# Performance work log

Measured on AMD Instinct MI355X. Metric: run time of the kernel, lower is better.

## Reference

```python
import jax, jax.numpy as jnp
import numpy as np
from math import ceil, log2

LEVELS = 8
# pywt 'db4' filters (length 8)
DB4_DEC_HI = np.array([-0.23037781330885523, 0.7148465705525415, -0.6308807679295904,
                       -0.02798376941698385, 0.18703481171888114, 0.030841381835986965,
                       -0.032883011666982945, -0.010597401784997278], dtype=np.float32)
DB4_REC_HI = np.array([-0.010597401784997278, -0.032883011666982945, 0.030841381835986965,
                       0.18703481171888114, -0.02798376941698385, -0.6308807679295904,
                       0.7148465705525415, -0.23037781330885523], dtype=np.float32)


def setup_inputs() -> dict:
    key = jax.random.key(0)
    x = jax.random.normal(key, (2048, 3000), dtype=jnp.float32)
    scaling = jnp.tile(jnp.asarray(DB4_DEC_HI), (LEVELS, 1))       # [levels, 8]
    scaling_rec = jnp.tile(jnp.asarray(DB4_REC_HI), (LEVELS, 1))   # [levels, 8]
    return {"input": x, "scaling": scaling, "scaling_rec": scaling_rec}


def _make_wavelet(h):
    # g = flip(h); g[1::2] *= -1
    g = jnp.flip(h, axis=-1)
    signs = jnp.where(jnp.arange(g.shape[-1]) % 2 == 1, -1.0, 1.0).astype(g.dtype)
    return g * signs


def _circ_conv(x, filt, transpose=False):
    # FFT-based circular convolution (filter zero-padded to input length)
    L = x.shape[-1]
    ra = jnp.fft.rfft(x)
    rb = jnp.fft.rfft(filt, n=L)
    if transpose:
        rb = jnp.conj(rb)
    return jnp.fft.irfft(ra * rb, n=L)


def _upsample2(x):
    # interleave zeros: out[:, ::2] = x
    n, k = x.shape
    out = jnp.zeros((n, 2 * k), dtype=x.dtype)
    return out.at[:, ::2].set(x)


def _forward(x, scaling, scaling_rec):
    levels = scaling.shape[0]
    m = x.shape[1]
    L = 2 ** ceil(log2(m))
    p0 = (L - m) // 2
    p1 = ceil((L - m) / 2)
    x = jnp.pad(x, ((0, 0), (p0, p1)), mode="edge")  # ReplicationPad1d

    approx = x
    wav_coeffs = []
    for lvl in range(levels):
        wavelet = _make_wavelet(scaling_rec[lvl])
        details = _circ_conv(approx, wavelet)[:, ::2]
        approx = _circ_conv(approx, scaling[lvl])[:, ::2]
        wav_coeffs.append(details)
    wav_coeffs.append(approx)

    # (no thresholding: the original forward copies coeffs unmodified)
    filtered = list(wav_coeffs)
    approx = filtered[-1]
    for lvl in reversed(range(levels)):
        details = filtered[lvl]
        wav_syn = _make_wavelet(scaling_rec[lvl])
        d_rec = _circ_conv(_upsample2(details), wav_syn, transpose=True)
        a_rec = _circ_conv(_upsample2(approx), scaling[lvl], transpose=True)
        approx = d_rec + a_rec

    recon = approx[:, p0:m + p1]
    coeffs = jnp.concatenate(wav_coeffs, axis=-1)  # total length == L
    return recon, coeffs


def reference(input, scaling, scaling_rec):
    return _forward(input, scaling, scaling_rec)
```

## Files before the change

### kernel.cpp

```cpp
#include <hip/hip_runtime.h>

#define NROWS 2048
#define MLEN  3000
#define LPAD  4096
#define PAD0  548
#define NLVL  8
#define NT    256

__global__ __launch_bounds__(NT) void despawn_kernel(
    const float* __restrict__ x,
    const float* __restrict__ scaling,
    const float* __restrict__ scaling_rec,
    float* __restrict__ recon_out,
    float* __restrict__ coef_out)
{
    __shared__ float SA[LPAD];
    __shared__ float SB[LPAD / 2];
    __shared__ float fsca[NLVL * 8];
    __shared__ float fwav[NLVL * 8];

    const int tid = threadIdx.x;
    const int row = blockIdx.x;
    float* const crow = coef_out + (size_t)row * LPAD;

    if (tid < NLVL * 8) {
        const int lvl = tid >> 3, k = tid & 7;
        fsca[tid] = scaling[tid];
        fwav[tid] = scaling_rec[lvl * 8 + (7 - k)] * ((k & 1) ? -1.0f : 1.0f);
    }

    const float* xr = x + (size_t)row * MLEN;
    for (int i = tid; i < LPAD; i += NT) {
        int j = i - PAD0;
        j = j < 0 ? 0 : (j > MLEN - 1 ? MLEN - 1 : j);
        SA[((i & 1) ? (LPAD / 2) : 0) + (i >> 1)] = xr[j];
    }
    __syncthreads();

    float* cur = SA;
    float* alt = SB;
    int M = LPAD;
    int coff = 0;
    for (int lvl = 0; lvl < NLVL; ++lvl) {
        const int H = M >> 1;
        const int hm = H - 1;
        const float* we = &fwav[lvl * 8];
        const float* se = &fsca[lvl * 8];
        const float* ev = cur;
        const float* od = cur + H;
        for (int j = tid; j < H; j += NT) {
            float ds = 0.0f, as = 0.0f;
#pragma unroll
            for (int m = 0; m < 4; ++m) {
                const float vE = ev[(j - m) & hm];
                const float vO = od[(j - m - 1) & hm];
                ds = fmaf(vE, we[2 * m], ds);
                ds = fmaf(vO, we[2 * m + 1], ds);
                as = fmaf(vE, se[2 * m], as);
                as = fmaf(vO, se[2 * m + 1], as);
            }
            crow[coff + j] = ds;
            alt[((j & 1) ? (H >> 1) : 0) + (j >> 1)] = as;
        }
        __syncthreads();
        coff += H;
        float* t = cur; cur = alt; alt = t;
        M = H;
    }
    if (tid < 16) {
        const float v = cur[((tid & 1) ? 8 : 0) + (tid >> 1)];
        crow[LPAD - 16 + tid] = v;
        SA[16 + tid] = v;
    }
    __syncthreads();

    const float* a = SA + 16;
    int len = 16;
    float* obuf = SB;
    for (int lvl = NLVL - 1; lvl >= 0; --lvl) {
        const int Mout = len << 1;
        const int lmask = len - 1;
        const float* d = crow + (LPAD - (LPAD >> lvl));
        const float* we = &fwav[lvl * 8];
        const float* se = &fsca[lvl * 8];
        for (int n = tid; n < Mout; n += NT) {
            const int p = n & 1;
            const int i0 = (n + p) >> 1;
            float sum = 0.0f;
#pragma unroll
            for (int m = 0; m < 4; ++m) {
                const int idx = (i0 + m) & lmask;
                sum = fmaf(d[idx], we[p + 2 * m], sum);
                sum = fmaf(a[idx], se[p + 2 * m], sum);
            }
            obuf[n] = sum;
        }
        __syncthreads();
        a = obuf;
        len = Mout;
        obuf = (obuf == SB) ? SA : SB;
    }

    float* ro = recon_out + (size_t)row * MLEN;
    for (int i = tid; i < MLEN; i += NT) ro[i] = a[PAD0 + i];
}

extern "C" void kernel_launch(void* const* d_in, const int* in_sizes, int n_in,
                              void* d_out, int out_size, void* d_ws, size_t ws_size,
                              hipStream_t stream) {
    const float* x           = (const float*)d_in[0];
    const float* scaling     = (const float*)d_in[1];
    const float* scaling_rec = (const float*)d_in[2];
    float* recon = (float*)d_out;
    float* coefo = recon + (size_t)NROWS * MLEN;
    despawn_kernel<<<dim3(NROWS), dim3(NT), 0, stream>>>(x, scaling, scaling_rec,
                                                         recon, coefo);
    (void)in_sizes; (void)n_in; (void)out_size; (void)d_ws; (void)ws_size;
}
```

Measured before the change: 113.8 us.

## Vectorize wavelet levels with float4 and cache coarse details in LDS

The input load, each analysis level and each synthesis level now work on four or eight outputs per thread using float4 loads and stores, with the filter taps held in registers. Detail coefficients for levels 3 and above are also kept in a shared-memory buffer, so synthesis reads them from LDS rather than from global memory. The last synthesis level writes straight to the recon output with vectorized stores, dropping the extra staging pass. The aim is fewer LDS and global transactions and less per-element index arithmetic, at the cost of more registers and an extra 2KB of LDS per block.

```diff
diff --git a/kernel.cpp b/kernel.cpp
--- a/kernel.cpp
+++ b/kernel.cpp
@@ -6,6 +6,8 @@
 #define PAD0  548
 #define NLVL  8
 #define NT    256
+
+union F4 { float4 v; float f[4]; };
 
 __global__ __launch_bounds__(NT) void despawn_kernel(
     const float* __restrict__ x,
@@ -14,95 +16,185 @@
     float* __restrict__ recon_out,
     float* __restrict__ coef_out)
 {
-    __shared__ float SA[LPAD];
-    __shared__ float SB[LPAD / 2];
-    __shared__ float fsca[NLVL * 8];
-    __shared__ float fwav[NLVL * 8];
+    __shared__ __align__(16) float SA[LPAD];
+    __shared__ __align__(16) float SB[LPAD / 2];
+    __shared__ __align__(16) float CS[512];
+    __shared__ float fsca[64];
+    __shared__ float fwav[64];
 
     const int tid = threadIdx.x;
     const int row = blockIdx.x;
     float* const crow = coef_out + (size_t)row * LPAD;
 
-    if (tid < NLVL * 8) {
+    if (tid < 64) {
         const int lvl = tid >> 3, k = tid & 7;
         fsca[tid] = scaling[tid];
         fwav[tid] = scaling_rec[lvl * 8 + (7 - k)] * ((k & 1) ? -1.0f : 1.0f);
     }
 
     const float* xr = x + (size_t)row * MLEN;
-    for (int i = tid; i < LPAD; i += NT) {
-        int j = i - PAD0;
-        j = j < 0 ? 0 : (j > MLEN - 1 ? MLEN - 1 : j);
-        SA[((i & 1) ? (LPAD / 2) : 0) + (i >> 1)] = xr[j];
+    const float xlo = xr[0], xhi = xr[MLEN - 1];
+    {
+        const float4* xr4 = reinterpret_cast<const float4*>(xr);
+        for (int g = tid; g < MLEN / 4; g += NT) {
+            F4 u; u.v = xr4[g];
+            const int h = PAD0 / 2 + 2 * g;
+            *reinterpret_cast<float2*>(&SA[h])            = make_float2(u.f[0], u.f[2]);
+            *reinterpret_cast<float2*>(&SA[LPAD / 2 + h]) = make_float2(u.f[1], u.f[3]);
+        }
+    }
+    for (int i = tid; i < PAD0 / 2; i += NT) {
+        SA[i] = xlo;
+        SA[LPAD / 2 + i] = xlo;
+        SA[PAD0 / 2 + MLEN / 2 + i] = xhi;
+        SA[LPAD / 2 + PAD0 / 2 + MLEN / 2 + i] = xhi;
     }
     __syncthreads();
 
-    float* cur = SA;
-    float* alt = SB;
-    int M = LPAD;
-    int coff = 0;
-    for (int lvl = 0; lvl < NLVL; ++lvl) {
-        const int H = M >> 1;
-        const int hm = H - 1;
-        const float* we = &fwav[lvl * 8];
-        const float* se = &fsca[lvl * 8];
-        const float* ev = cur;
-        const float* od = cur + H;
-        for (int j = tid; j < H; j += NT) {
-            float ds = 0.0f, as = 0.0f;
-#pragma unroll
-            for (int m = 0; m < 4; ++m) {
-                const float vE = ev[(j - m) & hm];
-                const float vO = od[(j - m - 1) & hm];
-                ds = fmaf(vE, we[2 * m], ds);
-                ds = fmaf(vO, we[2 * m + 1], ds);
-                as = fmaf(vE, se[2 * m], as);
-                as = fmaf(vO, se[2 * m + 1], as);
-            }
-            crow[coff + j] = ds;
-            alt[((j & 1) ? (H >> 1) : 0) + (j >> 1)] = as;
-        }
-        __syncthreads();
-        coff += H;
-        float* t = cur; cur = alt; alt = t;
-        M = H;
-    }
+    {
+        float* cur = SA;
+        float* alt = SB;
+        int H = LPAD / 2;
+        int coff = 0;
+        for (int lvl = 0; lvl < NLVL; ++lvl) {
+            float W[8], S[8];
+#pragma unroll
+            for (int k = 0; k < 8; ++k) { W[k] = fwav[lvl * 8 + k]; S[k] = fsca[lvl * 8 + k]; }
+            const int q = H >> 2;
+            const int qm = q - 1;
+            const float4* ev4 = reinterpret_cast<const float4*>(cur);
+            const float4* od4 = reinterpret_cast<const float4*>(cur + H);
+            float4* dst4 = reinterpret_cast<float4*>(crow + coff);
+            float4* cs4 = (lvl >= 3) ? reinterpret_cast<float4*>(&CS[coff - 3584]) : nullptr;
+            for (int t = tid; t < q; t += NT) {
+                F4 Ea, Eb, Oa, Ob;
+                Ea.v = ev4[(t - 1) & qm];
+                Eb.v = ev4[t];
+                Oa.v = od4[(t - 1) & qm];
+                Ob.v = od4[t];
+                float e[8] = {Ea.f[0],Ea.f[1],Ea.f[2],Ea.f[3],Eb.f[0],Eb.f[1],Eb.f[2],Eb.f[3]};
+                float o[8] = {Oa.f[0],Oa.f[1],Oa.f[2],Oa.f[3],Ob.f[0],Ob.f[1],Ob.f[2],Ob.f[3]};
+                float ds[4], as[4];
+#pragma unroll
+                for (int u = 0; u < 4; ++u) {
+                    float d = 0.f, a = 0.f;
+#pragma unroll
+                    for (int m = 0; m < 4; ++m) {
+                        const float vE = e[4 + u - m];
+                        const float vO = o[3 + u - m];
+                        d = fmaf(vE, W[2 * m], d);
+                        d = fmaf(vO, W[2 * m + 1], d);
+                        a = fmaf(vE, S[2 * m], a);
+                        a = fmaf(vO, S[2 * m + 1], a);
+                    }
+                    ds[u] = d; as[u] = a;
+                }
+                F4 dv; dv.f[0] = ds[0]; dv.f[1] = ds[1]; dv.f[2] = ds[2]; dv.f[3] = ds[3];
+                dst4[t] = dv.v;
+                if (cs4) cs4[t] = dv.v;
+                *reinterpret_cast<float2*>(alt + 2 * t)            = make_float2(as[0], as[2]);
+                *reinterpret_cast<float2*>(alt + (H >> 1) + 2 * t) = make_float2(as[1], as[3]);
+            }
+            __syncthreads();
+            coff += H;
+            float* tmp = cur; cur = alt; alt = tmp;
+            H >>= 1;
+        }
+    }
+
     if (tid < 16) {
-        const float v = cur[((tid & 1) ? 8 : 0) + (tid >> 1)];
+        const float v = SA[((tid & 1) ? 8 : 0) + (tid >> 1)];
         crow[LPAD - 16 + tid] = v;
-        SA[16 + tid] = v;
+        CS[496 + tid] = v;
     }
     __syncthreads();
 
-    const float* a = SA + 16;
+    const float* a = &CS[496];
+    float* obuf = SB;
     int len = 16;
-    float* obuf = SB;
-    for (int lvl = NLVL - 1; lvl >= 0; --lvl) {
+    for (int lvl = NLVL - 1; lvl >= 1; --lvl) {
+        float W[8], S[8];
+#pragma unroll
+        for (int k = 0; k < 8; ++k) { W[k] = fwav[lvl * 8 + k]; S[k] = fsca[lvl * 8 + k]; }
         const int Mout = len << 1;
-        const int lmask = len - 1;
-        const float* d = crow + (LPAD - (LPAD >> lvl));
-        const float* we = &fwav[lvl * 8];
-        const float* se = &fsca[lvl * 8];
-        for (int n = tid; n < Mout; n += NT) {
-            const int p = n & 1;
-            const int i0 = (n + p) >> 1;
-            float sum = 0.0f;
-#pragma unroll
-            for (int m = 0; m < 4; ++m) {
-                const int idx = (i0 + m) & lmask;
-                sum = fmaf(d[idx], we[p + 2 * m], sum);
-                sum = fmaf(a[idx], se[p + 2 * m], sum);
-            }
-            obuf[n] = sum;
+        const int doff = LPAD - (LPAD >> lvl);
+        const float4* d4 = (lvl >= 3)
+            ? reinterpret_cast<const float4*>(&CS[doff - 3584])
+            : reinterpret_cast<const float4*>(crow + doff);
+        const float4* a4 = reinterpret_cast<const float4*>(a);
+        const int gq = Mout >> 3;
+        const int fm = (len >> 2) - 1;
+        for (int g = tid; g < gq; g += NT) {
+            F4 Da, Db, Aa, Ab;
+            Da.v = d4[g]; Db.v = d4[(g + 1) & fm];
+            Aa.v = a4[g]; Ab.v = a4[(g + 1) & fm];
+            float dd[8] = {Da.f[0],Da.f[1],Da.f[2],Da.f[3],Db.f[0],Db.f[1],Db.f[2],Db.f[3]};
+            float aa[8] = {Aa.f[0],Aa.f[1],Aa.f[2],Aa.f[3],Ab.f[0],Ab.f[1],Ab.f[2],Ab.f[3]};
+            float out[8];
+#pragma unroll
+            for (int u = 0; u < 8; ++u) {
+                const int p = u & 1, c = (u + 1) >> 1;
+                float s = 0.f;
+#pragma unroll
+                for (int m = 0; m < 4; ++m) {
+                    s = fmaf(dd[c + m], W[p + 2 * m], s);
+                    s = fmaf(aa[c + m], S[p + 2 * m], s);
+                }
+                out[u] = s;
+            }
+            F4 o0, o1;
+            o0.f[0] = out[0]; o0.f[1] = out[1]; o0.f[2] = out[2]; o0.f[3] = out[3];
+            o1.f[0] = out[4]; o1.f[1] = out[5]; o1.f[2] = out[6]; o1.f[3] = out[7];
+            float4* ob4 = reinterpret_cast<float4*>(obuf + 8 * g);
+            ob4[0] = o0.v; ob4[1] = o1.v;
         }
         __syncthreads();
         a = obuf;
+        obuf = (obuf == SB) ? SA : SB;
         len = Mout;
-        obuf = (obuf == SB) ? SA : SB;
-    }
-
-    float* ro = recon_out + (size_t)row * MLEN;
-    for (int i = tid; i < MLEN; i += NT) ro[i] = a[PAD0 + i];
+    }
+    {
+        float W[8], S[8];
+#pragma unroll
+        for (int k = 0; k < 8; ++k) { W[k] = fwav[k]; S[k] = fsca[k]; }
+        const float4* d4 = reinterpret_cast<const float4*>(crow);
+        const float4* a4 = reinterpret_cast<const float4*>(a);
+        const int fm = (len >> 2) - 1;
+        float* const ro = recon_out + (size_t)row * MLEN;
+        for (int g = tid; g < (LPAD >> 3); g += NT) {
+            F4 Da, Db, Aa, Ab;
+            Da.v = d4[g]; Db.v = d4[(g + 1) & fm];
+            Aa.v = a4[g]; Ab.v = a4[(g + 1) & fm];
+            float dd[8] = {Da.f[0],Da.f[1],Da.f[2],Da.f[3],Db.f[0],Db.f[1],Db.f[2],Db.f[3]};
+            float aa[8] = {Aa.f[0],Aa.f[1],Aa.f[2],Aa.f[3],Ab.f[0],Ab.f[1],Ab.f[2],Ab.f[3]};
+            float out[8];
+#pragma unroll
+            for (int u = 0; u < 8; ++u) {
+                const int p = u & 1, c = (u + 1) >> 1;
+                float s = 0.f;
+#pragma unroll
+                for (int m = 0; m < 4; ++m) {
+                    s = fmaf(dd[c + m], W[p + 2 * m], s);
+                    s = fmaf(aa[c + m], S[p + 2 * m], s);
+                }
+                out[u] = s;
+            }
+            const int n0 = 8 * g;
+            if (n0 >= PAD0 && n0 + 8 <= PAD0 + MLEN) {
+                F4 o0, o1;
+                o0.f[0] = out[0]; o0.f[1] = out[1]; o0.f[2] = out[2]; o0.f[3] = out[3];
+                o1.f[0] = out[4]; o1.f[1] = out[5]; o1.f[2] = out[6]; o1.f[3] = out[7];
+                float4* r4 = reinterpret_cast<float4*>(ro + (n0 - PAD0));
+                r4[0] = o0.v; r4[1] = o1.v;
+            } else {
+#pragma unroll
+                for (int u = 0; u < 8; ++u) {
+                    const int n = n0 + u;
+                    if (n >= PAD0 && n < PAD0 + MLEN) ro[n - PAD0] = out[u];
+                }
+            }
+        }
+    }
 }
 
 extern "C" void kernel_launch(void* const* d_in, const int* in_sizes, int n_in,
```

Result: faster. 99.58 us (-12.5%).
